# Kernel optimization log

Measured on AMD Instinct MI355X. Metric: run time of the kernel, lower is better.

## Reference

```python
import jax, jax.numpy as jnp
import numpy as np

B, S, D, H = 2, 2048, 1024, 16
DEPTH = D // H
NEG = -1e9


def setup_inputs() -> dict:
    key = jax.random.key(0)
    ks = jax.random.split(key, 8)
    scale = 1.0 / np.sqrt(D)
    inp = {
        "query": jax.random.normal(ks[0], (B, S, D), jnp.float32),
        "key": jax.random.normal(ks[1], (B, S, D), jnp.float32),
        "value": jax.random.normal(ks[2], (B, S, D), jnp.float32),
        # causal look-ahead mask: 1 where attention is disallowed
        "mask": (1.0 - jnp.tril(jnp.ones((S, S), jnp.float32)))[None, None, :, :],
        "Wq": jax.random.normal(ks[3], (D, D), jnp.float32) * scale,
        "Wk": jax.random.normal(ks[4], (D, D), jnp.float32) * scale,
        "Wv": jax.random.normal(ks[5], (D, D), jnp.float32) * scale,
        "Wo": jax.random.normal(ks[6], (D, D), jnp.float32) * scale,
        "bq": jnp.zeros((D,), jnp.float32),
        "bk": jnp.zeros((D,), jnp.float32),
        "bv": jnp.zeros((D,), jnp.float32),
        "bo": jnp.zeros((D,), jnp.float32),
    }
    return inp


def _split_heads(x):
    # [B,S,D] -> [B,H,S,depth]
    return x.reshape(B, -1, H, DEPTH).transpose(0, 2, 1, 3)


def reference(query, key, value, mask, Wq, Wk, Wv, Wo, bq, bk, bv, bo):
    q = _split_heads(query @ Wq + bq)
    k = _split_heads(key @ Wk + bk)
    v = _split_heads(value @ Wv + bv)
    logits = jnp.einsum("bhqd,bhkd->bhqk", q, k) / jnp.sqrt(jnp.float32(DEPTH))
    logits = logits + mask * NEG
    attn = jax.nn.softmax(logits, axis=-1)
    ctx = jnp.einsum("bhqk,bhkd->bhqd", attn, v)  # [B,H,S,depth]
    concat = ctx.transpose(0, 2, 1, 3).reshape(B, -1, D)
    return concat @ Wo + bo
```

## Files before the change

### kernel.cpp

```cpp
#include <hip/hip_runtime.h>
#include <hip/hip_bf16.h>
#include <stdint.h>

#define BB 2
#define SS 2048
#define DDIM 1024
#define HH 16
#define DEPTH 64
#define MROWS (BB*SS)

typedef short bf16x8 __attribute__((ext_vector_type(8)));
typedef float f32x4 __attribute__((ext_vector_type(4)));

__device__ inline ushort f2bf(float f) {
  union { float f; unsigned u; } v; v.f = f;
  unsigned r = v.u + 0x7fffu + ((v.u >> 16) & 1u);
  return (ushort)(r >> 16);
}

__device__ inline uint pkbf(float a, float b) {
  uint r;
  asm("v_cvt_pk_bf16_f32 %0, %1, %2" : "=v"(r) : "v"(a), "v"(b));
  return r;
}

__device__ inline void gload_lds16(const void* g, void* l) {
  __builtin_amdgcn_global_load_lds(
      (const __attribute__((address_space(1))) unsigned*)g,
      (__attribute__((address_space(3))) unsigned*)l,
      16, 0, 0);
}

__global__ void prep_kernel(const float* __restrict__ q, const float* __restrict__ k,
                            const float* __restrict__ v,
                            ushort* __restrict__ xq, ushort* __restrict__ xk,
                            ushort* __restrict__ xv,
                            const float* __restrict__ W0, const float* __restrict__ W1,
                            const float* __restrict__ W2, const float* __restrict__ W3,
                            ushort* __restrict__ T0, ushort* __restrict__ T1,
                            ushort* __restrict__ T2, ushort* __restrict__ T3) {
  __shared__ float tile[32][33];
  if (blockIdx.x < 6144) {
    int z = blockIdx.x >> 11;
    const float* in = (z == 0) ? q : (z == 1) ? k : v;
    ushort* out = (z == 0) ? xq : (z == 1) ? xk : xv;
    int i = (blockIdx.x & 2047) * 256 + threadIdx.x;
    const float4* p = (const float4*)in + (size_t)i * 2;
    float4 a = p[0], b = p[1];
    uint tmp[4] = { pkbf(a.x, a.y), pkbf(a.z, a.w), pkbf(b.x, b.y), pkbf(b.z, b.w) };
    *(uint4*)(out + (size_t)i * 8) = *(uint4*)tmp;
  } else {
    int idx = blockIdx.x - 6144;
    int z = idx >> 10;
    int rr = idx & 1023;
    const float* W = (z == 0) ? W0 : (z == 1) ? W1 : (z == 2) ? W2 : W3;
    ushort* T = (z == 0) ? T0 : (z == 1) ? T1 : (z == 2) ? T2 : T3;
    int tx = threadIdx.x & 31, ty = threadIdx.x >> 5;
    int n0 = (rr & 31) * 32, k0 = (rr >> 5) * 32;
#pragma unroll
    for (int i = 0; i < 4; i++)
      tile[ty + i * 8][tx] = W[(size_t)(k0 + ty + i * 8) * DDIM + n0 + tx];
    __syncthreads();
#pragma unroll
    for (int i = 0; i < 4; i++)
      T[(size_t)(n0 + ty + i * 8) * DDIM + k0 + tx] = f2bf(tile[tx][ty + i * 8]);
  }
}

__global__ __launch_bounds__(256) void qkv_gemm_kernel(
    const ushort* __restrict__ Xq, const ushort* __restrict__ Xk, const ushort* __restrict__ Xv,
    const ushort* __restrict__ Wqt, const ushort* __restrict__ Wkt, const ushort* __restrict__ Wvt,
    const float* __restrict__ bqp, const float* __restrict__ bkp, const float* __restrict__ bvp,
    ushort* __restrict__ Qh, ushort* __restrict__ Kh, ushort* __restrict__ Vtg) {
  const int id = blockIdx.x;
  const int xcd = id & 7;
  const int rest = id >> 3;
  const int xblk = rest & 7;
  const int slot = rest >> 3;
  const int g = xcd * 12 + slot;
  const int yblk = g & 31;
  const int z = g >> 5;

  const ushort* A  = (z == 0) ? Xq  : (z == 1) ? Xk  : Xv;
  const ushort* Bt = (z == 0) ? Wqt : (z == 1) ? Wkt : Wvt;
  const float* bias = (z == 0) ? bqp : (z == 1) ? bkp : bvp;
  const int K = DDIM;

  __shared__ __align__(16) ushort As[128 * 32];
  __shared__ __align__(16) ushort Bs[128 * 32];
  const int tid = threadIdx.x;
  const int w = tid >> 6, lane = tid & 63;
  const int m0 = yblk * 128, n0 = xblk * 128;
  const int wr = (w >> 1) * 64, wc = (w & 1) * 64;
  const int l4 = lane >> 4, l15 = lane & 15;
  const int srow = lane >> 2;
  const int scol = (lane & 3) * 8;

  f32x4 zero = {0.f, 0.f, 0.f, 0.f};
  f32x4 acc[4][4];
#pragma unroll
  for (int i = 0; i < 4; i++)
#pragma unroll
    for (int j = 0; j < 4; j++) acc[i][j] = zero;

  for (int k0 = 0; k0 < K; k0 += 32) {
#pragma unroll
    for (int it = 0; it < 2; ++it) {
      int r = it * 64 + w * 16;
      gload_lds16(A + (size_t)(m0 + r + srow) * K + k0 + scol, &As[r * 32]);
      gload_lds16(Bt + (size_t)(n0 + r + srow) * K + k0 + scol, &Bs[r * 32]);
    }
    __syncthreads();
    bf16x8 af[4], bfr[4];
#pragma unroll
    for (int m = 0; m < 4; m++)
      af[m] = *(const bf16x8*)&As[(wr + m * 16 + l15) * 32 + l4 * 8];
#pragma unroll
    for (int n = 0; n < 4; n++)
      bfr[n] = *(const bf16x8*)&Bs[(wc + n * 16 + l15) * 32 + l4 * 8];
#pragma unroll
    for (int m = 0; m < 4; m++)
#pragma unroll
      for (int n = 0; n < 4; n++)
        acc[m][n] = __builtin_amdgcn_mfma_f32_16x16x32_bf16(af[m], bfr[n], acc[m][n], 0, 0, 0);
    __syncthreads();
  }

  if (z != 2) {
    ushort* outp = (z == 0) ? Qh : Kh;
#pragma unroll
    for (int m = 0; m < 4; m++) {
#pragma unroll
      for (int n = 0; n < 4; n++) {
        int col = n0 + wc + n * 16 + l15;
        float bv = bias[col];
        int hh = col >> 6, dd = col & 63;
#pragma unroll
        for (int r = 0; r < 4; r++) {
          int row = m0 + wr + m * 16 + l4 * 4 + r;
          int bb = row >> 11, s = row & (SS - 1);
          outp[((size_t)(bb * HH + hh) * SS + s) * DEPTH + dd] = f2bf(acc[m][n][r] + bv);
        }
      }
    }
  } else {
    ushort* wtile = (w < 2) ? &As[w * 2048] : &Bs[(w - 2) * 2048];
    const int gcol0 = n0 + wc;
    const int hh = gcol0 >> 6;
    const int bb = m0 >> 11;
    const int s0g = (m0 + wr) & (SS - 1);
#pragma unroll
    for (int p = 0; p < 2; ++p) {
#pragma unroll
      for (int nn = 0; nn < 2; ++nn) {
        int n = p * 2 + nn;
        int dloc = nn * 16 + l15;
        float bv = bias[gcol0 + p * 32 + dloc];
#pragma unroll
        for (int m = 0; m < 4; m++) {
#pragma unroll
          for (int rr = 0; rr < 4; rr += 2) {
            int sloc = m * 16 + l4 * 4 + rr;
            int gg = (sloc >> 3) ^ (dloc & 7);
            uint pk = pkbf(acc[m][n][rr] + bv, acc[m][n][rr + 1] + bv);
            *(uint*)&wtile[dloc * 64 + gg * 8 + (sloc & 7)] = pk;
          }
        }
      }
      __syncthreads();
#pragma unroll
      for (int i = 0; i < 4; ++i) {
        int dloc = (lane >> 3) + i * 8;
        int gg = (lane & 7) ^ (dloc & 7);
        bf16x8 val = *(const bf16x8*)&wtile[dloc * 64 + gg * 8];
        int dglob = p * 32 + dloc;
        size_t addr = ((size_t)(bb * HH + hh) * DEPTH + dglob) * SS + s0g + (lane & 7) * 8;
        *(bf16x8*)&Vtg[addr] = val;
      }
      __syncthreads();
    }
  }
}

__global__ __launch_bounds__(256, 2) void out_gemm_kernel(
    const ushort* __restrict__ A, const ushort* __restrict__ Bt,
    const float* __restrict__ bias, float* __restrict__ out,
    int M, int N, int K) {
  __shared__ __align__(16) ushort As[128 * 32];
  __shared__ __align__(16) ushort Bs[64 * 32];
  const int id = blockIdx.x;
  const int xcd = id & 7;
  const int rest = id >> 3;
  const int xblk = rest & 15;
  const int slot = rest >> 4;
  const int yblk = xcd * 4 + slot;

  const int tid = threadIdx.x;
  const int w = tid >> 6, lane = tid & 63;
  const int m0 = yblk * 128, n0 = xblk * 64;
  const int wr = (w >> 1) * 64, wc = (w & 1) * 32;
  const int l4 = lane >> 4, l15 = lane & 15;
  const int srow = lane >> 2;
  const int scol = (lane & 3) * 8;

  f32x4 zero = {0.f, 0.f, 0.f, 0.f};
  f32x4 acc[4][2];
#pragma unroll
  for (int i = 0; i < 4; i++)
#pragma unroll
    for (int j = 0; j < 2; j++) acc[i][j] = zero;

  for (int k0 = 0; k0 < K; k0 += 32) {
#pragma unroll
    for (int it = 0; it < 2; ++it) {
      int r = it * 64 + w * 16;
      gload_lds16(A + (size_t)(m0 + r + srow) * K + k0 + scol, &As[r * 32]);
    }
    gload_lds16(Bt + (size_t)(n0 + w * 16 + srow) * K + k0 + scol, &Bs[(w * 16) * 32]);
    __syncthreads();
    bf16x8 af[4], bfr[2];
#pragma unroll
    for (int m = 0; m < 4; m++)
      af[m] = *(const bf16x8*)&As[(wr + m * 16 + l15) * 32 + l4 * 8];
#pragma unroll
    for (int n = 0; n < 2; n++)
      bfr[n] = *(const bf16x8*)&Bs[(wc + n * 16 + l15) * 32 + l4 * 8];
#pragma unroll
    for (int m = 0; m < 4; m++)
#pragma unroll
      for (int n = 0; n < 2; n++)
        acc[m][n] = __builtin_amdgcn_mfma_f32_16x16x32_bf16(af[m], bfr[n], acc[m][n], 0, 0, 0);
    __syncthreads();
  }

#pragma unroll
  for (int m = 0; m < 4; m++) {
#pragma unroll
    for (int n = 0; n < 2; n++) {
      int col = n0 + wc + n * 16 + l15;
      float bv = bias[col];
#pragma unroll
      for (int r = 0; r < 4; r++) {
        int row = m0 + wr + m * 16 + l4 * 4 + r;
        out[(size_t)row * N + col] = acc[m][n][r] + bv;
      }
    }
  }
}

__global__ __launch_bounds__(256, 4) void attn_kernel(
    const ushort* __restrict__ Qh, const ushort* __restrict__ Kh,
    const ushort* __restrict__ Vt, ushort* __restrict__ ctx) {
  __shared__ __align__(16) ushort Ks[2][64 * 64];
  __shared__ __align__(16) ushort Vs[2][64 * 64];
  __shared__ __align__(16) ushort Ps[4][16 * 64];
  const int tid = threadIdx.x;
  const int w = tid >> 6, lane = tid & 63;
  const int l4 = lane >> 4, l15 = lane & 15;
  const float CE = 0.18033688f;

  const int xcd = blockIdx.x & 7;
  const int local = blockIdx.x >> 3;
  const int bh = xcd * 4 + (local & 3);
  const int chunk = 31 - (local >> 2);
  const int b = bh >> 4, h = bh & 15;
  const size_t qkbase = (size_t)bh * SS * DEPTH;
  const size_t vbase  = (size_t)bh * DEPTH * SS;

  const int srow_w = w * 8 + (lane >> 3);
  const int colb_lin = (lane & 7) * 16;
  const int swz_rd = (l15 & 7) << 3;

  const int q0 = chunk * 64 + w * 16;
  const int nt = chunk + 1;

  bf16x8 aq[2];
#pragma unroll
  for (int cc = 0; cc < 2; cc++)
    aq[cc] = *(const bf16x8*)&Qh[qkbase + (size_t)(q0 + l15) * DEPTH + cc * 32 + l4 * 8];

  f32x4 zero = {0.f, 0.f, 0.f, 0.f};
  f32x4 o[4];
  float m_run = -__builtin_inff(), l_run = 0.f;
#pragma unroll
  for (int d = 0; d < 4; d++) o[d] = zero;

  int buf = 0;
#pragma unroll
  for (int it = 0; it < 2; ++it) {
    int row = it * 32 + srow_w;
    int col_e = (colb_lin ^ ((row & 7) << 4)) >> 1;
    int ldsoff = it * 2048 + w * 512;
    gload_lds16(Kh + qkbase + (size_t)row * DEPTH + col_e, &Ks[0][ldsoff]);
    gload_lds16(Vt + vbase + (size_t)row * SS + col_e, &Vs[0][ldsoff]);
  }
  __syncthreads();

  for (int t = 0; t < nt; ++t) {
    if (t + 1 < nt) {
      const int kv1 = (t + 1) * 64;
#pragma unroll
      for (int it = 0; it < 2; ++it) {
        int row = it * 32 + srow_w;
        int col_e = (colb_lin ^ ((row & 7) << 4)) >> 1;
        int ldsoff = it * 2048 + w * 512;
        gload_lds16(Kh + qkbase + (size_t)(kv1 + row) * DEPTH + col_e, &Ks[buf ^ 1][ldsoff]);
        gload_lds16(Vt + vbase + (size_t)row * SS + kv1 + col_e, &Vs[buf ^ 1][ldsoff]);
      }
    }

    const int kv0 = t * 64;
    f32x4 s[4];
    __builtin_amdgcn_s_setprio(1);
#pragma unroll
    for (int n = 0; n < 4; n++) {
      f32x4 zacc = zero;
      int kr = n * 16 + l15;
#pragma unroll
      for (int cc = 0; cc < 2; cc++) {
        bf16x8 bk = *(const bf16x8*)&Ks[buf][kr * 64 + ((cc * 32 + l4 * 8) ^ swz_rd)];
        zacc = __builtin_amdgcn_mfma_f32_16x16x32_bf16(bk, aq[cc], zacc, 0, 0, 0);
      }
      s[n] = zacc;
    }
    __builtin_amdgcn_s_setprio(0);

    const int qg = q0 + l15;
    if (t == nt - 1) {
#pragma unroll
      for (int n = 0; n < 4; n++) {
        int kb = kv0 + n * 16 + l4 * 4;
#pragma unroll
        for (int r = 0; r < 4; r++)
          if (kb + r > qg) s[n][r] = -1e9f;
      }
    }

    float mx = -__builtin_inff();
#pragma unroll
    for (int n = 0; n < 4; n++)
      mx = fmaxf(mx, fmaxf(fmaxf(s[n][0], s[n][1]), fmaxf(s[n][2], s[n][3])));
    mx = fmaxf(mx, __shfl_xor(mx, 16));
    mx = fmaxf(mx, __shfl_xor(mx, 32));
    if (!__all(mx - m_run <= 44.36f)) {
      float mnew = fmaxf(m_run, mx);
      float alpha = exp2f((m_run - mnew) * CE);
      m_run = mnew;
      l_run *= alpha;
#pragma unroll
      for (int d = 0; d < 4; d++) o[d] *= alpha;
    }
    float mc = m_run * CE;
    float rs = 0.f;
#pragma unroll
    for (int n = 0; n < 4; n++)
#pragma unroll
      for (int r = 0; r < 4; r++) {
        float p = exp2f(s[n][r] * CE - mc);
        s[n][r] = p;
        rs += p;
      }
    l_run += rs;

    ushort* Pw = &Ps[w][0];
#pragma unroll
    for (int n = 0; n < 4; n++) {
      int col = (n * 16 + l4 * 4) ^ swz_rd;
      *(uint*)&Pw[l15 * 64 + col]     = pkbf(s[n][0], s[n][1]);
      *(uint*)&Pw[l15 * 64 + col + 2] = pkbf(s[n][2], s[n][3]);
    }

    bf16x8 pa[2];
#pragma unroll
    for (int cc = 0; cc < 2; cc++)
      pa[cc] = *(const bf16x8*)&Pw[l15 * 64 + ((cc * 32 + l4 * 8) ^ swz_rd)];

    __builtin_amdgcn_s_setprio(1);
#pragma unroll
    for (int d = 0; d < 4; d++) {
      int dr = d * 16 + l15;
#pragma unroll
      for (int cc = 0; cc < 2; cc++) {
        bf16x8 av = *(const bf16x8*)&Vs[buf][dr * 64 + ((cc * 32 + l4 * 8) ^ swz_rd)];
        o[d] = __builtin_amdgcn_mfma_f32_16x16x32_bf16(av, pa[cc], o[d], 0, 0, 0);
      }
    }
    __builtin_amdgcn_s_setprio(0);

    __syncthreads();
    buf ^= 1;
  }

  float lv = l_run;
  lv += __shfl_xor(lv, 16);
  lv += __shfl_xor(lv, 32);
  float inv = 1.f / lv;
  size_t rowbase = ((size_t)(b * SS + q0 + l15)) * DDIM + h * DEPTH;
#pragma unroll
  for (int d = 0; d < 4; d++) {
    *(uint*)&ctx[rowbase + d * 16 + l4 * 4]     = pkbf(o[d][0] * inv, o[d][1] * inv);
    *(uint*)&ctx[rowbase + d * 16 + l4 * 4 + 2] = pkbf(o[d][2] * inv, o[d][3] * inv);
  }
}

extern "C" void kernel_launch(void* const* d_in, const int* in_sizes, int n_in,
                              void* d_out, int out_size, void* d_ws, size_t ws_size,
                              hipStream_t stream) {
  const float* query = (const float*)d_in[0];
  const float* key_  = (const float*)d_in[1];
  const float* value = (const float*)d_in[2];
  const float* Wq = (const float*)d_in[4];
  const float* Wk = (const float*)d_in[5];
  const float* Wv = (const float*)d_in[6];
  const float* Wo = (const float*)d_in[7];
  const float* bq = (const float*)d_in[8];
  const float* bk = (const float*)d_in[9];
  const float* bv = (const float*)d_in[10];
  const float* bo = (const float*)d_in[11];

  char* ws = (char*)d_ws;
  const size_t MB = 1u << 20;
  ushort* Xq  = (ushort*)(ws + 0 * MB);
  ushort* Xk  = (ushort*)(ws + 8 * MB);
  ushort* Xv  = (ushort*)(ws + 16 * MB);
  ushort* Wqt = (ushort*)(ws + 24 * MB);
  ushort* Wkt = (ushort*)(ws + 26 * MB);
  ushort* Wvt = (ushort*)(ws + 28 * MB);
  ushort* Wot = (ushort*)(ws + 30 * MB);
  ushort* Qh  = (ushort*)(ws + 32 * MB);
  ushort* Kh  = (ushort*)(ws + 40 * MB);
  ushort* Vtg = (ushort*)(ws + 48 * MB);
  ushort* Cb  = (ushort*)(ws + 56 * MB);

  prep_kernel<<<6144 + 4096, 256, 0, stream>>>(query, key_, value, Xq, Xk, Xv,
                                               Wq, Wk, Wv, Wo, Wqt, Wkt, Wvt, Wot);

  qkv_gemm_kernel<<<768, 256, 0, stream>>>(
      Xq, Xk, Xv, Wqt, Wkt, Wvt, bq, bk, bv, Qh, Kh, Vtg);

  attn_kernel<<<1024, 256, 0, stream>>>(Qh, Kh, Vtg, Cb);

  out_gemm_kernel<<<512, 256, 0, stream>>>(
      Cb, Wot, bo, (float*)d_out, MROWS, DDIM, DDIM);
}
```

Before: 128.1 us.

## Fuse fp32-to-bf16 activation conversion into QKV GEMM and widen K tiles

Drops the separate activation conversion pass: the QKV GEMM now loads fp32 inputs into registers, converts them to bf16 while storing to LDS, and prefetches the next K-slice during compute. Both GEMMs move from 32-wide to 64-wide K tiles, which halves the number of barrier iterations. Q/K output stores are staged through a swizzled LDS tile so they can be written as 16-byte vectors. In exchange there is more register pressure from prefetching 8 float4s per thread, a launch_bounds occupancy hint of 3, and more LDS per block.

Result: faster. 118.2 us (-7.8%).

```diff
diff --git a/kernel.cpp b/kernel.cpp
--- a/kernel.cpp
+++ b/kernel.cpp
@@ -31,44 +31,28 @@
       16, 0, 0);
 }
 
-__global__ void prep_kernel(const float* __restrict__ q, const float* __restrict__ k,
-                            const float* __restrict__ v,
-                            ushort* __restrict__ xq, ushort* __restrict__ xk,
-                            ushort* __restrict__ xv,
-                            const float* __restrict__ W0, const float* __restrict__ W1,
-                            const float* __restrict__ W2, const float* __restrict__ W3,
-                            ushort* __restrict__ T0, ushort* __restrict__ T1,
-                            ushort* __restrict__ T2, ushort* __restrict__ T3) {
+__global__ void wprep_kernel(const float* __restrict__ W0, const float* __restrict__ W1,
+                             const float* __restrict__ W2, const float* __restrict__ W3,
+                             ushort* __restrict__ T0, ushort* __restrict__ T1,
+                             ushort* __restrict__ T2, ushort* __restrict__ T3) {
   __shared__ float tile[32][33];
-  if (blockIdx.x < 6144) {
-    int z = blockIdx.x >> 11;
-    const float* in = (z == 0) ? q : (z == 1) ? k : v;
-    ushort* out = (z == 0) ? xq : (z == 1) ? xk : xv;
-    int i = (blockIdx.x & 2047) * 256 + threadIdx.x;
-    const float4* p = (const float4*)in + (size_t)i * 2;
-    float4 a = p[0], b = p[1];
-    uint tmp[4] = { pkbf(a.x, a.y), pkbf(a.z, a.w), pkbf(b.x, b.y), pkbf(b.z, b.w) };
-    *(uint4*)(out + (size_t)i * 8) = *(uint4*)tmp;
-  } else {
-    int idx = blockIdx.x - 6144;
-    int z = idx >> 10;
-    int rr = idx & 1023;
-    const float* W = (z == 0) ? W0 : (z == 1) ? W1 : (z == 2) ? W2 : W3;
-    ushort* T = (z == 0) ? T0 : (z == 1) ? T1 : (z == 2) ? T2 : T3;
-    int tx = threadIdx.x & 31, ty = threadIdx.x >> 5;
-    int n0 = (rr & 31) * 32, k0 = (rr >> 5) * 32;
-#pragma unroll
-    for (int i = 0; i < 4; i++)
-      tile[ty + i * 8][tx] = W[(size_t)(k0 + ty + i * 8) * DDIM + n0 + tx];
-    __syncthreads();
-#pragma unroll
-    for (int i = 0; i < 4; i++)
-      T[(size_t)(n0 + ty + i * 8) * DDIM + k0 + tx] = f2bf(tile[tx][ty + i * 8]);
-  }
-}
-
-__global__ __launch_bounds__(256) void qkv_gemm_kernel(
-    const ushort* __restrict__ Xq, const ushort* __restrict__ Xk, const ushort* __restrict__ Xv,
+  int z = blockIdx.x >> 10;
+  int rr = blockIdx.x & 1023;
+  const float* W = (z == 0) ? W0 : (z == 1) ? W1 : (z == 2) ? W2 : W3;
+  ushort* T = (z == 0) ? T0 : (z == 1) ? T1 : (z == 2) ? T2 : T3;
+  int tx = threadIdx.x & 31, ty = threadIdx.x >> 5;
+  int n0 = (rr & 31) * 32, k0 = (rr >> 5) * 32;
+#pragma unroll
+  for (int i = 0; i < 4; i++)
+    tile[ty + i * 8][tx] = W[(size_t)(k0 + ty + i * 8) * DDIM + n0 + tx];
+  __syncthreads();
+#pragma unroll
+  for (int i = 0; i < 4; i++)
+    T[(size_t)(n0 + ty + i * 8) * DDIM + k0 + tx] = f2bf(tile[tx][ty + i * 8]);
+}
+
+__global__ __launch_bounds__(256, 3) void qkv_gemm_kernel(
+    const float* __restrict__ Aq, const float* __restrict__ Ak, const float* __restrict__ Av,
     const ushort* __restrict__ Wqt, const ushort* __restrict__ Wkt, const ushort* __restrict__ Wvt,
     const float* __restrict__ bqp, const float* __restrict__ bkp, const float* __restrict__ bvp,
     ushort* __restrict__ Qh, ushort* __restrict__ Kh, ushort* __restrict__ Vtg) {
@@ -81,20 +65,21 @@
   const int yblk = g & 31;
   const int z = g >> 5;
 
-  const ushort* A  = (z == 0) ? Xq  : (z == 1) ? Xk  : Xv;
+  const float*  Ap = (z == 0) ? Aq  : (z == 1) ? Ak  : Av;
   const ushort* Bt = (z == 0) ? Wqt : (z == 1) ? Wkt : Wvt;
   const float* bias = (z == 0) ? bqp : (z == 1) ? bkp : bvp;
-  const int K = DDIM;
-
-  __shared__ __align__(16) ushort As[128 * 32];
-  __shared__ __align__(16) ushort Bs[128 * 32];
+
+  __shared__ __align__(16) ushort As[128 * 64];
+  __shared__ __align__(16) ushort Bs[128 * 64];
   const int tid = threadIdx.x;
   const int w = tid >> 6, lane = tid & 63;
   const int m0 = yblk * 128, n0 = xblk * 128;
   const int wr = (w >> 1) * 64, wc = (w & 1) * 64;
   const int l4 = lane >> 4, l15 = lane & 15;
-  const int srow = lane >> 2;
-  const int scol = (lane & 3) * 8;
+  const int row16 = tid >> 4;
+  const int col4 = (tid & 15) * 4;
+  const int srow8 = w * 8 + (lane >> 3);
+  const int scol8 = (lane & 7) * 8;
 
   f32x4 zero = {0.f, 0.f, 0.f, 0.f};
   f32x4 acc[4][4];
@@ -103,45 +88,73 @@
 #pragma unroll
     for (int j = 0; j < 4; j++) acc[i][j] = zero;
 
-  for (int k0 = 0; k0 < K; k0 += 32) {
-#pragma unroll
-    for (int it = 0; it < 2; ++it) {
-      int r = it * 64 + w * 16;
-      gload_lds16(A + (size_t)(m0 + r + srow) * K + k0 + scol, &As[r * 32]);
-      gload_lds16(Bt + (size_t)(n0 + r + srow) * K + k0 + scol, &Bs[r * 32]);
+  float4 areg[8];
+#pragma unroll
+  for (int j = 0; j < 8; ++j)
+    areg[j] = *(const float4*)&Ap[(size_t)(m0 + j * 16 + row16) * DDIM + col4];
+
+  for (int t = 0; t < 16; ++t) {
+#pragma unroll
+    for (int it = 0; it < 4; ++it)
+      gload_lds16(Bt + (size_t)(n0 + it * 32 + srow8) * DDIM + t * 64 + scol8,
+                  &Bs[(it * 32 + w * 8) * 64]);
+#pragma unroll
+    for (int j = 0; j < 8; ++j) {
+      uint2 pk;
+      pk.x = pkbf(areg[j].x, areg[j].y);
+      pk.y = pkbf(areg[j].z, areg[j].w);
+      *(uint2*)&As[(j * 16 + row16) * 64 + col4] = pk;
     }
     __syncthreads();
-    bf16x8 af[4], bfr[4];
-#pragma unroll
-    for (int m = 0; m < 4; m++)
-      af[m] = *(const bf16x8*)&As[(wr + m * 16 + l15) * 32 + l4 * 8];
-#pragma unroll
-    for (int n = 0; n < 4; n++)
-      bfr[n] = *(const bf16x8*)&Bs[(wc + n * 16 + l15) * 32 + l4 * 8];
-#pragma unroll
-    for (int m = 0; m < 4; m++)
+    if (t + 1 < 16) {
+#pragma unroll
+      for (int j = 0; j < 8; ++j)
+        areg[j] = *(const float4*)&Ap[(size_t)(m0 + j * 16 + row16) * DDIM + (t + 1) * 64 + col4];
+    }
+#pragma unroll
+    for (int kk = 0; kk < 2; ++kk) {
+      bf16x8 af[4], bfr[4];
+#pragma unroll
+      for (int m = 0; m < 4; m++)
+        af[m] = *(const bf16x8*)&As[(wr + m * 16 + l15) * 64 + kk * 32 + l4 * 8];
 #pragma unroll
       for (int n = 0; n < 4; n++)
-        acc[m][n] = __builtin_amdgcn_mfma_f32_16x16x32_bf16(af[m], bfr[n], acc[m][n], 0, 0, 0);
+        bfr[n] = *(const bf16x8*)&Bs[(wc + n * 16 + l15) * 64 + kk * 32 + l4 * 8];
+#pragma unroll
+      for (int m = 0; m < 4; m++)
+#pragma unroll
+        for (int n = 0; n < 4; n++)
+          acc[m][n] = __builtin_amdgcn_mfma_f32_16x16x32_bf16(af[m], bfr[n], acc[m][n], 0, 0, 0);
+    }
     __syncthreads();
   }
 
   if (z != 2) {
     ushort* outp = (z == 0) ? Qh : Kh;
+    ushort* wtile = (w < 2) ? &As[w * 4096] : &Bs[(w - 2) * 4096];
+    const int gcol0 = n0 + wc;
+    const int hh = gcol0 >> 6;
+    const int bb = m0 >> 11;
+    const int s0g = (m0 + wr) & (SS - 1);
 #pragma unroll
     for (int m = 0; m < 4; m++) {
 #pragma unroll
       for (int n = 0; n < 4; n++) {
-        int col = n0 + wc + n * 16 + l15;
-        float bv = bias[col];
-        int hh = col >> 6, dd = col & 63;
+        int dloc = n * 16 + l15;
+        float bv = bias[gcol0 + dloc];
 #pragma unroll
         for (int r = 0; r < 4; r++) {
-          int row = m0 + wr + m * 16 + l4 * 4 + r;
-          int bb = row >> 11, s = row & (SS - 1);
-          outp[((size_t)(bb * HH + hh) * SS + s) * DEPTH + dd] = f2bf(acc[m][n][r] + bv);
+          int sloc = m * 16 + l4 * 4 + r;
+          wtile[sloc * 64 + (dloc ^ ((sloc & 7) << 3))] = f2bf(acc[m][n][r] + bv);
         }
       }
+    }
+#pragma unroll
+    for (int i = 0; i < 8; ++i) {
+      int srow = i * 8 + (lane >> 3);
+      int dch = (lane & 7) * 8;
+      bf16x8 val = *(const bf16x8*)&wtile[srow * 64 + (dch ^ ((srow & 7) << 3))];
+      *(bf16x8*)&outp[((size_t)(bb * HH + hh) * SS + s0g + srow) * DEPTH + dch] = val;
     }
   } else {
     ushort* wtile = (w < 2) ? &As[w * 2048] : &Bs[(w - 2) * 2048];
@@ -186,8 +199,8 @@
     const ushort* __restrict__ A, const ushort* __restrict__ Bt,
     const float* __restrict__ bias, float* __restrict__ out,
     int M, int N, int K) {
-  __shared__ __align__(16) ushort As[128 * 32];
-  __shared__ __align__(16) ushort Bs[64 * 32];
+  __shared__ __align__(16) ushort As[128 * 64];
+  __shared__ __align__(16) ushort Bs[64 * 64];
   const int id = blockIdx.x;
   const int xcd = id & 7;
   const int rest = id >> 3;
@@ -200,8 +213,8 @@
   const int m0 = yblk * 128, n0 = xblk * 64;
   const int wr = (w >> 1) * 64, wc = (w & 1) * 32;
   const int l4 = lane >> 4, l15 = lane & 15;
-  const int srow = lane >> 2;
-  const int scol = (lane & 3) * 8;
+  const int srow8 = w * 8 + (lane >> 3);
+  const int scol8 = (lane & 7) * 8;
 
   f32x4 zero = {0.f, 0.f, 0.f, 0.f};
   f32x4 acc[4][2];
@@ -210,26 +223,31 @@
 #pragma unroll
     for (int j = 0; j < 2; j++) acc[i][j] = zero;
 
-  for (int k0 = 0; k0 < K; k0 += 32) {
-#pragma unroll
-    for (int it = 0; it < 2; ++it) {
-      int r = it * 64 + w * 16;
-      gload_lds16(A + (size_t)(m0 + r + srow) * K + k0 + scol, &As[r * 32]);
-    }
-    gload_lds16(Bt + (size_t)(n0 + w * 16 + srow) * K + k0 + scol, &Bs[(w * 16) * 32]);
+  for (int t = 0; t < 16; ++t) {
+#pragma unroll
+    for (int it = 0; it < 4; ++it)
+      gload_lds16(A + (size_t)(m0 + it * 32 + srow8) * K + t * 64 + scol8,
+                  &As[(it * 32 + w * 8) * 64]);
+#pragma unroll
+    for (int it = 0; it < 2; ++it)
+      gload_lds16(Bt + (size_t)(n0 + it * 32 + srow8) * K + t * 64 + scol8,
+                  &Bs[(it * 32 + w * 8) * 64]);
     __syncthreads();
-    bf16x8 af[4], bfr[2];
-#pragma unroll
-    for (int m = 0; m < 4; m++)
-      af[m] = *(const bf16x8*)&As[(wr + m * 16 + l15) * 32 + l4 * 8];
-#pragma unroll
-    for (int n = 0; n < 2; n++)
-      bfr[n] = *(const bf16x8*)&Bs[(wc + n * 16 + l15) * 32 + l4 * 8];
-#pragma unroll
-    for (int m = 0; m < 4; m++)
+#pragma unroll
+    for (int kk = 0; kk < 2; ++kk) {
+      bf16x8 af[4], bfr[2];
+#pragma unroll
+      for (int m = 0; m < 4; m++)
+        af[m] = *(const bf16x8*)&As[(wr + m * 16 + l15) * 64 + kk * 32 + l4 * 8];
 #pragma unroll
       for (int n = 0; n < 2; n++)
-        acc[m][n] = __builtin_amdgcn_mfma_f32_16x16x32_bf16(af[m], bfr[n], acc[m][n], 0, 0, 0);
+        bfr[n] = *(const bf16x8*)&Bs[(wc + n * 16 + l15) * 64 + kk * 32 + l4 * 8];
+#pragma unroll
+      for (int m = 0; m < 4; m++)
+#pragma unroll
+        for (int n = 0; n < 2; n++)
+          acc[m][n] = __builtin_amdgcn_mfma_f32_16x16x32_bf16(af[m], bfr[n], acc[m][n], 0, 0, 0);
+    }
     __syncthreads();
   }
 
@@ -420,9 +438,6 @@
 
   char* ws = (char*)d_ws;
   const size_t MB = 1u << 20;
-  ushort* Xq  = (ushort*)(ws + 0 * MB);
-  ushort* Xk  = (ushort*)(ws + 8 * MB);
-  ushort* Xv  = (ushort*)(ws + 16 * MB);
   ushort* Wqt = (ushort*)(ws + 24 * MB);
   ushort* Wkt = (ushort*)(ws + 26 * MB);
   ushort* Wvt = (ushort*)(ws + 28 * MB);
@@ -432,11 +447,10 @@
   ushort* Vtg = (ushort*)(ws + 48 * MB);
   ushort* Cb  = (ushort*)(ws + 56 * MB);
 
-  prep_kernel<<<6144 + 4096, 256, 0, stream>>>(query, key_, value, Xq, Xk, Xv,
-                                               Wq, Wk, Wv, Wo, Wqt, Wkt, Wvt, Wot);
+  wprep_kernel<<<4096, 256, 0, stream>>>(Wq, Wk, Wv, Wo, Wqt, Wkt, Wvt, Wot);
 
   qkv_gemm_kernel<<<768, 256, 0, stream>>>(
-      Xq, Xk, Xv, Wqt, Wkt, Wvt, bq, bk, bv, Qh, Kh, Vtg);
+      query, key_, value, Wqt, Wkt, Wvt, bq, bk, bv, Qh, Kh, Vtg);
 
   attn_kernel<<<1024, 256, 0, stream>>>(Qh, Kh, Vtg, Cb);
 
```
